# Optimization experiments

Hardware: AMD Instinct MI355X
Metric: run time of the kernel (lower is better)

Reference implementation:

```python
import jax, jax.numpy as jnp
import numpy as np

N_HEADS = 16
N_KV_HEADS = 4
N_EMBD = 1024

def setup_inputs() -> dict:
    key = jax.random.key(0)
    kx, kq, kk, kv, ko = jax.random.split(key, 5)
    B, S, E = 2, 2048, N_EMBD
    head_dim = E // N_HEADS
    kv_dim = N_KV_HEADS * head_dim  # 256
    scale = 0.02
    return {
        "x": jax.random.normal(kx, (B, S, E), dtype=jnp.float32),
        "Wq": jax.random.normal(kq, (E, E), dtype=jnp.float32) * scale,
        "Wk": jax.random.normal(kk, (E, kv_dim), dtype=jnp.float32) * scale,
        "Wv": jax.random.normal(kv, (E, kv_dim), dtype=jnp.float32) * scale,
        "Wo": jax.random.normal(ko, (E, E), dtype=jnp.float32) * scale,
    }

def reference(x, Wq, Wk, Wv, Wo):
    B, S, E = x.shape
    H, KV = N_HEADS, N_KV_HEADS
    D = E // H            # head_dim = 64
    R = H // KV           # query heads per kv head = 4
    inv_sqrt_d = 1.0 / (D ** 0.5)

    q = (x @ Wq).reshape(B, S, KV, R, D)   # group query heads by kv group
    k = (x @ Wk).reshape(B, S, KV, D)
    v = (x @ Wv).reshape(B, S, KV, D)

    # repeat_interleave(kv, R, dim=heads) == broadcast kv head g to query heads (g, r)
    scores = jnp.einsum('bqgrd,bkgd->bgrqk', q, k) * inv_sqrt_d  # [B,KV,R,S,S]
    causal = jnp.tril(jnp.ones((S, S), dtype=bool))
    scores = jnp.where(causal, scores, jnp.float32(-jnp.inf))
    attn = jax.nn.softmax(scores, axis=-1)

    out = jnp.einsum('bgrqk,bkgd->bqgrd', attn, v).reshape(B, S, E)
    return out @ Wo
```

## Files before the change

kernel.cpp:

```cpp
#include <hip/hip_runtime.h>
#include <hip/hip_bf16.h>

#define B_SZ   2
#define S_LEN  2048
#define E_DIM  1024
#define H_Q    16
#define H_KV   4
#define HD     64
#define KV_DIM 256
#define M_ROWS (B_SZ * S_LEN)
#define N_QT128 (S_LEN / 128)

typedef short bf16x4 __attribute__((ext_vector_type(4)));
typedef short bf16x8 __attribute__((ext_vector_type(8)));
typedef float f32x4  __attribute__((ext_vector_type(4)));
typedef unsigned u32x2 __attribute__((ext_vector_type(2)));

#define MFMA16x32(a, b, c) __builtin_amdgcn_mfma_f32_16x16x32_bf16(a, b, c, 0, 0, 0)

#if __has_builtin(__builtin_amdgcn_mfma_f32_16x16x16bf16_1k)
#define MFMA_PV(a, b, c) __builtin_amdgcn_mfma_f32_16x16x16bf16_1k(a, b, c, 0, 0, 0)
#elif __has_builtin(__builtin_amdgcn_mfma_f32_16x16x16_bf16)
#define MFMA_PV(a, b, c) __builtin_amdgcn_mfma_f32_16x16x16_bf16(a, b, c, 0, 0, 0)
#else
static __device__ inline f32x4 mfma_pv_asm(bf16x4 a, bf16x4 b, f32x4 c) {
    asm volatile("v_mfma_f32_16x16x16_bf16 %0, %1, %2, %0"
                 : "+v"(c) : "v"(a), "v"(b));
    return c;
}
#define MFMA_PV(a, b, c) mfma_pv_asm(a, b, c)
#endif

static __device__ __forceinline__ short f32_to_bf16(float f) {
    unsigned u = __builtin_bit_cast(unsigned, f);
    u += 0x7fffu + ((u >> 16) & 1u);
    return (short)(u >> 16);
}

static __device__ __forceinline__ unsigned pack2_trunc(float a, float b) {
    return __builtin_amdgcn_perm(__builtin_bit_cast(unsigned, b),
                                 __builtin_bit_cast(unsigned, a),
                                 0x07060302u);
}

static __device__ __forceinline__ void load_lds16(const short* g, short* l) {
    __builtin_amdgcn_global_load_lds(
        (const __attribute__((address_space(1))) void*)g,
        (__attribute__((address_space(3))) void*)l, 16, 0, 0);
}

__device__ __forceinline__ void transpose_body(const float* __restrict__ W,
                                               short* __restrict__ Wt,
                                               int K, int N, int bx, int by) {
    __shared__ float t[32][33];
    const int n0 = bx * 32, k0 = by * 32;
    const int tx = threadIdx.x & 31, ty = threadIdx.x >> 5;
#pragma unroll
    for (int i = 0; i < 32; i += 8)
        t[ty + i][tx] = W[(long)(k0 + ty + i) * N + n0 + tx];
    __syncthreads();
#pragma unroll
    for (int i = 0; i < 32; i += 8)
        Wt[(long)(n0 + ty + i) * K + k0 + tx] = f32_to_bf16(t[tx][ty + i]);
}

__global__ __launch_bounds__(256)
void prep(const float* __restrict__ x,
          const float* __restrict__ Wq, const float* __restrict__ Wk,
          const float* __restrict__ Wv, const float* __restrict__ Wo,
          short* __restrict__ xbf, short* __restrict__ Wqt,
          short* __restrict__ Wkt, short* __restrict__ Wvt,
          short* __restrict__ Wot) {
    const int bid = blockIdx.x;
    if (bid < 4096) {
        const int i = bid * 256 + threadIdx.x;
        float4 v = ((const float4*)x)[i];
        bf16x4 o;
        o[0] = f32_to_bf16(v.x); o[1] = f32_to_bf16(v.y);
        o[2] = f32_to_bf16(v.z); o[3] = f32_to_bf16(v.w);
        ((bf16x4*)xbf)[i] = o;
    } else if (bid < 5120) {
        const int r = bid - 4096;
        transpose_body(Wq, Wqt, E_DIM, E_DIM, r & 31, r >> 5);
    } else if (bid < 5376) {
        const int r = bid - 5120;
        transpose_body(Wk, Wkt, E_DIM, KV_DIM, r & 7, r >> 3);
    } else if (bid < 5632) {
        const int r = bid - 5376;
        transpose_body(Wv, Wvt, E_DIM, KV_DIM, r & 7, r >> 3);
    } else {
        const int r = bid - 5632;
        transpose_body(Wo, Wot, E_DIM, E_DIM, r & 31, r >> 5);
    }
}

__device__ __forceinline__ void gemm128x64(const short* __restrict__ Ab,
                                           const short* __restrict__ Btb,
                                           int K, short* As, short* Bs,
                                           f32x4 acc[2][4]) {
    const int tid  = threadIdx.x;
    const int wave = tid >> 6;
    const int lane = tid & 63;
    const int lq   = lane & 15;
    const int lg   = lane >> 4;
    const int srow = lane >> 3;
    const int scol = (lane & 7) * 8;

#pragma unroll
    for (int i = 0; i < 2; ++i)
#pragma unroll
        for (int j = 0; j < 4; ++j) acc[i][j] = (f32x4){0.f, 0.f, 0.f, 0.f};

    for (int k0 = 0; k0 < K; k0 += 64) {
        __syncthreads();
#pragma unroll
        for (int it = 0; it < 4; ++it) {
            const int m0 = wave * 32 + it * 8;
            load_lds16(Ab + (size_t)(m0 + srow) * K + k0 + scol, As + m0 * 64);
        }
#pragma unroll
        for (int it = 0; it < 2; ++it) {
            const int n0 = wave * 16 + it * 8;
            load_lds16(Btb + (size_t)(n0 + srow) * K + k0 + scol, Bs + n0 * 64);
        }
        __syncthreads();
#pragma unroll
        for (int ks = 0; ks < 2; ++ks) {
            bf16x8 af[2], bfr[4];
#pragma unroll
            for (int i = 0; i < 2; ++i)
                af[i] = *(const bf16x8*)
                    &As[(wave * 32 + i * 16 + lq) * 64 + ks * 32 + lg * 8];
#pragma unroll
            for (int j = 0; j < 4; ++j)
                bfr[j] = *(const bf16x8*)
                    &Bs[(j * 16 + lq) * 64 + ks * 32 + lg * 8];
#pragma unroll
            for (int i = 0; i < 2; ++i)
#pragma unroll
                for (int j = 0; j < 4; ++j)
                    acc[i][j] = MFMA16x32(af[i], bfr[j], acc[i][j]);
        }
    }
}

__global__ __launch_bounds__(256)
void qkv_gemm(const short* __restrict__ xbf,
              const short* __restrict__ Wqt, const short* __restrict__ Wkt,
              const short* __restrict__ Wvt,
              short* __restrict__ Qbf, short* __restrict__ Kbf,
              short* __restrict__ Vtg, float qscale) {
    __shared__ short As[128 * 64];
    __shared__ short Bs[64 * 64];
    const int nb = blockIdx.x;
    const int mb = blockIdx.y;
    const short* Bt;
    if (nb < 16)      Bt = Wqt + (size_t)nb * 64 * E_DIM;
    else if (nb < 20) Bt = Wkt + (size_t)(nb - 16) * 64 * E_DIM;
    else              Bt = Wvt + (size_t)(nb - 20) * 64 * E_DIM;

    f32x4 acc[2][4];
    gemm128x64(xbf + (size_t)mb * 128 * E_DIM, Bt, E_DIM, As, Bs, acc);

    const int lane = threadIdx.x & 63, wave = threadIdx.x >> 6;
    const int lq = lane & 15, lg = lane >> 4;

    if (nb < 20) {
        short* out; int ldc, ncol0; float alpha;
        if (nb < 16) { out = Qbf; ldc = E_DIM; ncol0 = nb * 64; alpha = qscale; }
        else { out = Kbf; ldc = KV_DIM; ncol0 = (nb - 16) * 64; alpha = 1.f; }
#pragma unroll
        for (int i = 0; i < 2; ++i)
#pragma unroll
            for (int r = 0; r < 4; ++r) {
                const size_t row =
                    (size_t)mb * 128 + wave * 32 + i * 16 + lg * 4 + r;
#pragma unroll
                for (int j = 0; j < 4; ++j)
                    out[row * ldc + ncol0 + j * 16 + lq] =
                        f32_to_bf16(acc[i][j][r] * alpha);
            }
    } else {
        const int gg = nb - 20;
#pragma unroll
        for (int i = 0; i < 2; ++i)
#pragma unroll
            for (int r = 0; r < 4; ++r) {
                const int row = mb * 128 + wave * 32 + i * 16 + lg * 4 + r;
                const int bb = row >> 11, s = row & 2047;
#pragma unroll
                for (int j = 0; j < 4; ++j) {
                    const int d = j * 16 + lq;
                    Vtg[((long)(gg * 2 + bb) * HD + d) * S_LEN + s] =
                        f32_to_bf16(acc[i][j][r]);
                }
            }
    }
}

__global__ __launch_bounds__(256)
void gemm_o(const short* __restrict__ Abf, const short* __restrict__ Wot,
            float* __restrict__ C) {
    __shared__ short As[128 * 64];
    __shared__ short Bs[64 * 64];
    const int nb = blockIdx.x;
    const int mb = blockIdx.y;
    f32x4 acc[2][4];
    gemm128x64(Abf + (size_t)mb * 128 * E_DIM,
               Wot + (size_t)nb * 64 * E_DIM, E_DIM, As, Bs, acc);

    const int lane = threadIdx.x & 63, wave = threadIdx.x >> 6;
    const int lq = lane & 15, lg = lane >> 4;
#pragma unroll
    for (int i = 0; i < 2; ++i)
#pragma unroll
        for (int r = 0; r < 4; ++r) {
            const size_t row =
                (size_t)mb * 128 + wave * 32 + i * 16 + lg * 4 + r;
#pragma unroll
            for (int j = 0; j < 4; ++j)
                C[row * E_DIM + nb * 64 + j * 16 + lq] = acc[i][j][r];
        }
}

struct KVregs { bf16x8 k[2], v[2]; };

__device__ __forceinline__ void stage_load(const short*& pK, const short*& pV,
                                           KVregs& kv) {
#pragma unroll
    for (int it = 0; it < 2; ++it) {
        kv.k[it] = *(const bf16x8*)(pK + (size_t)it * 32 * KV_DIM);
        kv.v[it] = *(const bf16x8*)(pV + (size_t)it * 32 * S_LEN);
    }
    pK += (size_t)64 * KV_DIM;
    pV += 64;
}

__device__ __forceinline__ void stage_write(short (*Ks)[72], short (*Vt)[72],
                                            const KVregs& kv) {
    const int tid = threadIdx.x;
#pragma unroll
    for (int it = 0; it < 2; ++it) {
        const int c   = tid + it * 256;
        const int row = c >> 3;
        const int ch  = c & 7;
        *(bf16x8*)&Ks[row][ch * 8] = kv.k[it];
        *(bf16x8*)&Vt[row][ch * 8] = kv.v[it];
    }
}

template <bool MASKED>
__device__ __forceinline__ void proc_tile(const short (*Ks)[72],
                                          const short (*Vt)[72],
                                          const bf16x8 (&qf)[2][2],
                                          int lq, int lg, int dd,
                                          f32x4 (&o)[2][4],
                                          f32x4 (&lsum)[2]) {
    f32x4 s[4][2];
    bool need[4][2];
#pragma unroll
    for (int c = 0; c < 4; ++c) {
        const int rel0 = c * 16 - dd;
        need[c][0] = !MASKED || (rel0 < 16);
        need[c][1] = !MASKED || (rel0 - 16 < 16);
        if (MASKED && !need[c][1]) continue;
        bf16x8 kf0 = *(const bf16x8*)&Ks[c * 16 + lq][lg * 8];
        bf16x8 kf1 = *(const bf16x8*)&Ks[c * 16 + lq][32 + lg * 8];
#pragma unroll
        for (int f = 0; f < 2; ++f) {
            if (MASKED && !need[c][f]) continue;
            f32x4 acc = (f32x4){0.f, 0.f, 0.f, 0.f};
            acc = MFMA16x32(kf0, qf[f][0], acc);
            acc = MFMA16x32(kf1, qf[f][1], acc);
            if (MASKED) {
                if (c * 16 - 16 * f - dd == 0) {
#pragma unroll
                    for (int r = 0; r < 4; ++r)
                        if (lg * 4 + r > lq) acc[r] = -INFINITY;
                }
            }
            s[c][f] = acc;
        }
    }

#pragma unroll
    for (int c = 0; c < 4; ++c)
#pragma unroll
        for (int f = 0; f < 2; ++f) {
            if (MASKED && !need[c][f]) continue;
#pragma unroll
            for (int r = 0; r < 4; ++r)
                s[c][f][r] = __builtin_amdgcn_exp2f(s[c][f][r]);
        }

    const bf16x4 ones4 = {(short)0x3F80, (short)0x3F80,
                          (short)0x3F80, (short)0x3F80};
#pragma unroll
    for (int c = 0; c < 4; ++c) {
        if (MASKED && !need[c][1]) continue;
        bf16x4 pa[2];
#pragma unroll
        for (int f = 0; f < 2; ++f) {
            if (MASKED && !need[c][f]) continue;
            u32x2 packed;
            packed[0] = pack2_trunc(s[c][f][0], s[c][f][1]);
            packed[1] = pack2_trunc(s[c][f][2], s[c][f][3]);
            pa[f] = __builtin_bit_cast(bf16x4, packed);
            lsum[f] = MFMA_PV(pa[f], ones4, lsum[f]);
        }
#pragma unroll
        for (int dc = 0; dc < 4; ++dc) {
            bf16x4 vf = *(const bf16x4*)&Vt[dc * 16 + lq][c * 16 + lg * 4];
#pragma unroll
            for (int f = 0; f < 2; ++f)
                if (!MASKED || need[c][f]) o[f][dc] = MFMA_PV(pa[f], vf, o[f][dc]);
        }
    }
}

__global__ __launch_bounds__(256)
void flash_mfma(const short* __restrict__ Qb,
                const short* __restrict__ Kb,
                const short* __restrict__ Vtg,
                float* __restrict__ Op,
                float* __restrict__ Lp) {
    const int pair  = blockIdx.x;
    const int h     = blockIdx.y;
    const int b     = blockIdx.z >> 1;
    const int split = blockIdx.z & 1;
    const int g     = h >> 2;

    const int tid  = threadIdx.x;
    const int wv   = tid >> 6;
    const int lane = tid & 63;
    const int lq   = lane & 15;
    const int lg   = lane >> 4;

    __shared__ short Ks[64][72];
    __shared__ short Vt[64][72];

    for (int rep = 0; rep < 2; ++rep) {
        const int QT = rep ? (N_QT128 - 1 - pair) : pair;
        const int Q0 = QT * 128;
        const int kt0 = split ? QT + 1 : 0;
        const int kt1 = split ? 2 * QT + 1 : QT;
        const int nmask = split ? ((QT >= 1) ? 2 : 1) : ((QT == 0) ? 1 : 0);
        const int qmin = Q0 + wv * 32;

        const short* qrow =
            Qb + ((long)(b * S_LEN + qmin + lq)) * E_DIM + h * HD;
        bf16x8 qf[2][2];
#pragma unroll
        for (int f = 0; f < 2; ++f) {
            qf[f][0] = *(const bf16x8*)(qrow + (long)f * 16 * E_DIM + lg * 8);
            qf[f][1] = *(const bf16x8*)(qrow + (long)f * 16 * E_DIM + 32 + lg * 8);
        }

        f32x4 o[2][4];
#pragma unroll
        for (int f = 0; f < 2; ++f)
#pragma unroll
            for (int dc = 0; dc < 4; ++dc) o[f][dc] = (f32x4){0.f, 0.f, 0.f, 0.f};
        f32x4 lsum[2];
        lsum[0] = lsum[1] = (f32x4){0.f, 0.f, 0.f, 0.f};

        const short* pK = Kb +
            ((long)b * S_LEN + (long)kt0 * 64 + (tid >> 3)) * KV_DIM +
            g * HD + (tid & 7) * 8;
        const short* pV = Vtg +
            ((long)(g * 2 + b) * HD + (tid >> 3)) * S_LEN +
            (long)kt0 * 64 + (tid & 7) * 8;

        KVregs kv;
        if (kt0 <= kt1) stage_load(pK, pV, kv);

        for (int kt = kt0; kt <= kt1; ++kt) {
            __syncthreads();
            stage_write(Ks, Vt, kv);
            __syncthreads();
            if (kt < kt1)
                stage_load(pK, pV, kv);

            if (kt <= kt1 - nmask) {
                proc_tile<false>(Ks, Vt, qf, lq, lg, 0, o, lsum);
            } else {
                const int dd = __builtin_amdgcn_readfirstlane(qmin - kt * 64);
                proc_tile<true>(Ks, Vt, qf, lq, lg, dd, o, lsum);
            }
        }

        const long ibase = (long)(split * 2 + b) << 21;
#pragma unroll
        for (int f = 0; f < 2; ++f)
#pragma unroll
            for (int r = 0; r < 4; ++r) {
                const long base = ibase +
                    ((long)(qmin + f * 16 + lg * 4 + r)) * E_DIM + h * HD + lq;
#pragma unroll
                for (int dc = 0; dc < 4; ++dc) Op[base + dc * 16] = o[f][dc][r];
            }
        if (lq == 0) {
#pragma unroll
            for (int f = 0; f < 2; ++f)
#pragma unroll
                for (int r = 0; r < 4; ++r)
                    Lp[((split * 2 + b) * H_Q + h) * S_LEN +
                       qmin + f * 16 + lg * 4 + r] = lsum[f][r];
        }
    }
}

__global__ __launch_bounds__(256)
void merge_o(const float* __restrict__ Op, const float* __restrict__ Lp,
             short* __restrict__ Abf) {
    const long idx4 = (long)blockIdx.x * 256 + threadIdx.x;
    const long e = idx4 * 4;
    const int b  = (int)(e >> 21);
    const long ei = e & ((1L << 21) - 1);
    const int s  = (int)(ei >> 10);
    const int hh = ((int)(ei & 1023)) >> 6;
    const float4 v0 = *(const float4*)(Op + ((long)(0 + b) << 21) + ei);
    const float4 v1 = *(const float4*)(Op + ((long)(2 + b) << 21) + ei);
    const float l = Lp[((0 + b) * H_Q + hh) * S_LEN + s] +
                    Lp[((2 + b) * H_Q + hh) * S_LEN + s];
    const float inv = 1.f / l;
    bf16x4 o;
    o[0] = f32_to_bf16((v0.x + v1.x) * inv);
    o[1] = f32_to_bf16((v0.y + v1.y) * inv);
    o[2] = f32_to_bf16((v0.z + v1.z) * inv);
    o[3] = f32_to_bf16((v0.w + v1.w) * inv);
    *(bf16x4*)(Abf + e) = o;
}

extern "C" void kernel_launch(void* const* d_in, const int* in_sizes, int n_in,
                              void* d_out, int out_size, void* d_ws, size_t ws_size,
                              hipStream_t stream) {
    const float* x  = (const float*)d_in[0];
    const float* Wq = (const float*)d_in[1];
    const float* Wk = (const float*)d_in[2];
    const float* Wv = (const float*)d_in[3];
    const float* Wo = (const float*)d_in[4];
    float* out = (float*)d_out;

    short* xbf = (short*)d_ws;
    short* Wqt = xbf + (size_t)M_ROWS * E_DIM;
    short* Wkt = Wqt + (size_t)E_DIM * E_DIM;
    short* Wvt = Wkt + (size_t)KV_DIM * E_DIM;
    short* Wot = Wvt + (size_t)KV_DIM * E_DIM;
    short* Qbf = Wot + (size_t)E_DIM * E_DIM;
    short* Kbf = Qbf + (size_t)M_ROWS * E_DIM;
    short* Vtg = Kbf + (size_t)M_ROWS * KV_DIM;
    short* Abf = Vtg + (size_t)8 * HD * S_LEN;
    float* Op  = (float*)(Abf + (size_t)M_ROWS * E_DIM);
    float* Lp  = Op + (size_t)4 * S_LEN * E_DIM;

    const float qscale = 0.125f * 1.44269504088896340736f;

    prep<<<dim3(6656), dim3(256), 0, stream>>>(
        x, Wq, Wk, Wv, Wo, xbf, Wqt, Wkt, Wvt, Wot);
    qkv_gemm<<<dim3(24, M_ROWS / 128), dim3(256), 0, stream>>>(
        xbf, Wqt, Wkt, Wvt, Qbf, Kbf, Vtg, qscale);
    flash_mfma<<<dim3(8, H_Q, 4), dim3(256), 0, stream>>>(
        Qbf, Kbf, Vtg, Op, Lp);
    merge_o<<<dim3(M_ROWS * E_DIM / 4 / 256), dim3(256), 0, stream>>>(
        Op, Lp, Abf);
    gemm_o<<<dim3(E_DIM / 64, M_ROWS / 128), dim3(256), 0, stream>>>(
        Abf, Wot, out);
}
```

Measured before the change: 165.3 us.

## Fuse split-KV merge into flash kernel via atomic completion counters

Measured after the change: 346.1 us. 109% more time.

```diff
diff --git a/kernel.cpp b/kernel.cpp
--- a/kernel.cpp
+++ b/kernel.cpp
@@ -70,7 +70,7 @@
           const float* __restrict__ Wv, const float* __restrict__ Wo,
           short* __restrict__ xbf, short* __restrict__ Wqt,
           short* __restrict__ Wkt, short* __restrict__ Wvt,
-          short* __restrict__ Wot) {
+          short* __restrict__ Wot, int* __restrict__ cnt) {
     const int bid = blockIdx.x;
     if (bid < 4096) {
         const int i = bid * 256 + threadIdx.x;
@@ -88,9 +88,12 @@
     } else if (bid < 5632) {
         const int r = bid - 5376;
         transpose_body(Wv, Wvt, E_DIM, KV_DIM, r & 7, r >> 3);
-    } else {
+    } else if (bid < 6656) {
         const int r = bid - 5632;
         transpose_body(Wo, Wot, E_DIM, E_DIM, r & 31, r >> 5);
+    } else {
+        cnt[threadIdx.x] = 0;
+        cnt[256 + threadIdx.x] = 0;
     }
 }
 
@@ -323,7 +326,9 @@
                 const short* __restrict__ Kb,
                 const short* __restrict__ Vtg,
                 float* __restrict__ Op,
-                float* __restrict__ Lp) {
+                float* __restrict__ Lp,
+                short* __restrict__ Abf,
+                int* __restrict__ cnt) {
     const int pair  = blockIdx.x;
     const int h     = blockIdx.y;
     const int b     = blockIdx.z >> 1;
@@ -338,6 +343,7 @@
 
     __shared__ short Ks[64][72];
     __shared__ short Vt[64][72];
+    __shared__ int oldv;
 
     for (int rep = 0; rep < 2; ++rep) {
         const int QT = rep ? (N_QT128 - 1 - pair) : pair;
@@ -407,29 +413,36 @@
                     Lp[((split * 2 + b) * H_Q + h) * S_LEN +
                        qmin + f * 16 + lg * 4 + r] = lsum[f][r];
         }
-    }
-}
-
-__global__ __launch_bounds__(256)
-void merge_o(const float* __restrict__ Op, const float* __restrict__ Lp,
-             short* __restrict__ Abf) {
-    const long idx4 = (long)blockIdx.x * 256 + threadIdx.x;
-    const long e = idx4 * 4;
-    const int b  = (int)(e >> 21);
-    const long ei = e & ((1L << 21) - 1);
-    const int s  = (int)(ei >> 10);
-    const int hh = ((int)(ei & 1023)) >> 6;
-    const float4 v0 = *(const float4*)(Op + ((long)(0 + b) << 21) + ei);
-    const float4 v1 = *(const float4*)(Op + ((long)(2 + b) << 21) + ei);
-    const float l = Lp[((0 + b) * H_Q + hh) * S_LEN + s] +
-                    Lp[((2 + b) * H_Q + hh) * S_LEN + s];
-    const float inv = 1.f / l;
-    bf16x4 o;
-    o[0] = f32_to_bf16((v0.x + v1.x) * inv);
-    o[1] = f32_to_bf16((v0.y + v1.y) * inv);
-    o[2] = f32_to_bf16((v0.z + v1.z) * inv);
-    o[3] = f32_to_bf16((v0.w + v1.w) * inv);
-    *(bf16x4*)(Abf + e) = o;
+
+        __threadfence();
+        __syncthreads();
+        if (tid == 0)
+            oldv = atomicAdd(&cnt[(b * H_Q + h) * N_QT128 + QT], 1);
+        __syncthreads();
+        if (oldv == 1) {
+            __threadfence();
+            const int os = 1 - split;
+            const long obase = (long)(os * 2 + b) << 21;
+#pragma unroll
+            for (int f = 0; f < 2; ++f)
+#pragma unroll
+                for (int r = 0; r < 4; ++r) {
+                    const int row = qmin + f * 16 + lg * 4 + r;
+                    const float lo =
+                        Lp[((os * 2 + b) * H_Q + h) * S_LEN + row];
+                    const float inv = 1.f / (lsum[f][r] + lo);
+                    const long gb = obase + (long)row * E_DIM + h * HD + lq;
+                    short* arow =
+                        Abf + ((long)(b * S_LEN + row)) * E_DIM + h * HD + lq;
+#pragma unroll
+                    for (int dc = 0; dc < 4; ++dc) {
+                        const float oo = Op[gb + dc * 16];
+                        arow[dc * 16] =
+                            f32_to_bf16((o[f][dc][r] + oo) * inv);
+                    }
+                }
+        }
+    }
 }
 
 extern "C" void kernel_launch(void* const* d_in, const int* in_sizes, int n_in,
@@ -453,17 +466,16 @@
     short* Abf = Vtg + (size_t)8 * HD * S_LEN;
     float* Op  = (float*)(Abf + (size_t)M_ROWS * E_DIM);
     float* Lp  = Op + (size_t)4 * S_LEN * E_DIM;
+    int*   cnt = (int*)(Lp + (size_t)4 * H_Q * S_LEN);
 
     const float qscale = 0.125f * 1.44269504088896340736f;
 
-    prep<<<dim3(6656), dim3(256), 0, stream>>>(
-        x, Wq, Wk, Wv, Wo, xbf, Wqt, Wkt, Wvt, Wot);
+    prep<<<dim3(6657), dim3(256), 0, stream>>>(
+        x, Wq, Wk, Wv, Wo, xbf, Wqt, Wkt, Wvt, Wot, cnt);
     qkv_gemm<<<dim3(24, M_ROWS / 128), dim3(256), 0, stream>>>(
         xbf, Wqt, Wkt, Wvt, Qbf, Kbf, Vtg, qscale);
     flash_mfma<<<dim3(8, H_Q, 4), dim3(256), 0, stream>>>(
-        Qbf, Kbf, Vtg, Op, Lp);
-    merge_o<<<dim3(M_ROWS * E_DIM / 4 / 256), dim3(256), 0, stream>>>(
-        Op, Lp, Abf);
+        Qbf, Kbf, Vtg, Op, Lp, Abf, cnt);
     gemm_o<<<dim3(E_DIM / 64, M_ROWS / 128), dim3(256), 0, stream>>>(
         Abf, Wot, out);
 }
```

## Drop LDS staging in flash attention; one-wave blocks load K/V from global

Applied to the files above, without the earlier changes.

Result: slower. 225.9 us (+36.6%).

```diff
diff --git a/kernel.cpp b/kernel.cpp
--- a/kernel.cpp
+++ b/kernel.cpp
@@ -223,35 +223,10 @@
         }
 }
 
-struct KVregs { bf16x8 k[2], v[2]; };
-
-__device__ __forceinline__ void stage_load(const short*& pK, const short*& pV,
-                                           KVregs& kv) {
-#pragma unroll
-    for (int it = 0; it < 2; ++it) {
-        kv.k[it] = *(const bf16x8*)(pK + (size_t)it * 32 * KV_DIM);
-        kv.v[it] = *(const bf16x8*)(pV + (size_t)it * 32 * S_LEN);
-    }
-    pK += (size_t)64 * KV_DIM;
-    pV += 64;
-}
-
-__device__ __forceinline__ void stage_write(short (*Ks)[72], short (*Vt)[72],
-                                            const KVregs& kv) {
-    const int tid = threadIdx.x;
-#pragma unroll
-    for (int it = 0; it < 2; ++it) {
-        const int c   = tid + it * 256;
-        const int row = c >> 3;
-        const int ch  = c & 7;
-        *(bf16x8*)&Ks[row][ch * 8] = kv.k[it];
-        *(bf16x8*)&Vt[row][ch * 8] = kv.v[it];
-    }
-}
 
 template <bool MASKED>
-__device__ __forceinline__ void proc_tile(const short (*Ks)[72],
-                                          const short (*Vt)[72],
+__device__ __forceinline__ void proc_tile(const short* __restrict__ pK,
+                                          const short* __restrict__ pV,
                                           const bf16x8 (&qf)[2][2],
                                           int lq, int lg, int dd,
                                           f32x4 (&o)[2][4],
@@ -264,8 +239,8 @@
         need[c][0] = !MASKED || (rel0 < 16);
         need[c][1] = !MASKED || (rel0 - 16 < 16);
         if (MASKED && !need[c][1]) continue;
-        bf16x8 kf0 = *(const bf16x8*)&Ks[c * 16 + lq][lg * 8];
-        bf16x8 kf1 = *(const bf16x8*)&Ks[c * 16 + lq][32 + lg * 8];
+        bf16x8 kf0 = *(const bf16x8*)(pK + (size_t)c * 16 * KV_DIM);
+        bf16x8 kf1 = *(const bf16x8*)(pK + (size_t)c * 16 * KV_DIM + 32);
 #pragma unroll
         for (int f = 0; f < 2; ++f) {
             if (MASKED && !need[c][f]) continue;
@@ -310,7 +285,8 @@
         }
 #pragma unroll
         for (int dc = 0; dc < 4; ++dc) {
-            bf16x4 vf = *(const bf16x4*)&Vt[dc * 16 + lq][c * 16 + lg * 4];
+            bf16x4 vf = *(const bf16x4*)
+                (pV + (size_t)dc * 16 * S_LEN + c * 16);
 #pragma unroll
             for (int f = 0; f < 2; ++f)
                 if (!MASKED || need[c][f]) o[f][dc] = MFMA_PV(pa[f], vf, o[f][dc]);
@@ -318,7 +294,7 @@
     }
 }
 
-__global__ __launch_bounds__(256)
+__global__ __launch_bounds__(64)
 void flash_mfma(const short* __restrict__ Qb,
                 const short* __restrict__ Kb,
                 const short* __restrict__ Vtg,
@@ -326,18 +302,15 @@
                 float* __restrict__ Lp) {
     const int pair  = blockIdx.x;
     const int h     = blockIdx.y;
-    const int b     = blockIdx.z >> 1;
-    const int split = blockIdx.z & 1;
+    const int zz    = blockIdx.z;
+    const int wv    = zz >> 2;
+    const int b     = (zz >> 1) & 1;
+    const int split = zz & 1;
     const int g     = h >> 2;
 
-    const int tid  = threadIdx.x;
-    const int wv   = tid >> 6;
-    const int lane = tid & 63;
+    const int lane = threadIdx.x;
     const int lq   = lane & 15;
     const int lg   = lane >> 4;
-
-    __shared__ short Ks[64][72];
-    __shared__ short Vt[64][72];
 
     for (int rep = 0; rep < 2; ++rep) {
         const int QT = rep ? (N_QT128 - 1 - pair) : pair;
@@ -365,28 +338,21 @@
         lsum[0] = lsum[1] = (f32x4){0.f, 0.f, 0.f, 0.f};
 
         const short* pK = Kb +
-            ((long)b * S_LEN + (long)kt0 * 64 + (tid >> 3)) * KV_DIM +
-            g * HD + (tid & 7) * 8;
+            ((long)b * S_LEN + (long)kt0 * 64 + lq) * KV_DIM +
+            g * HD + lg * 8;
         const short* pV = Vtg +
-            ((long)(g * 2 + b) * HD + (tid >> 3)) * S_LEN +
-            (long)kt0 * 64 + (tid & 7) * 8;
-
-        KVregs kv;
-        if (kt0 <= kt1) stage_load(pK, pV, kv);
+            ((long)(g * 2 + b) * HD + lq) * S_LEN +
+            (long)kt0 * 64 + lg * 4;
 
         for (int kt = kt0; kt <= kt1; ++kt) {
-            __syncthreads();
-            stage_write(Ks, Vt, kv);
-            __syncthreads();
-            if (kt < kt1)
-                stage_load(pK, pV, kv);
-
             if (kt <= kt1 - nmask) {
-                proc_tile<false>(Ks, Vt, qf, lq, lg, 0, o, lsum);
+                proc_tile<false>(pK, pV, qf, lq, lg, 0, o, lsum);
             } else {
                 const int dd = __builtin_amdgcn_readfirstlane(qmin - kt * 64);
-                proc_tile<true>(Ks, Vt, qf, lq, lg, dd, o, lsum);
+                proc_tile<true>(pK, pV, qf, lq, lg, dd, o, lsum);
             }
+            pK += (size_t)64 * KV_DIM;
+            pV += 64;
         }
 
         const long ibase = (long)(split * 2 + b) << 21;
@@ -460,7 +426,7 @@
         x, Wq, Wk, Wv, Wo, xbf, Wqt, Wkt, Wvt, Wot);
     qkv_gemm<<<dim3(24, M_ROWS / 128), dim3(256), 0, stream>>>(
         xbf, Wqt, Wkt, Wvt, Qbf, Kbf, Vtg, qscale);
-    flash_mfma<<<dim3(8, H_Q, 4), dim3(256), 0, stream>>>(
+    flash_mfma<<<dim3(8, H_Q, 16), dim3(64), 0, stream>>>(
         Qbf, Kbf, Vtg, Op, Lp);
     merge_o<<<dim3(M_ROWS * E_DIM / 4 / 256), dim3(256), 0, stream>>>(
         Op, Lp, Abf);
```
